# Optimization experiments

Hardware: AMD Instinct MI355X
Metric: run time of the kernel (lower is better)

## Reference

```python
import jax, jax.numpy as jnp
import numpy as np

B, H, W, C = 8, 64, 64, 512
C8, C2 = C // 8, C // 2  # f/g channels = 64, h channels = 256 (divisor = 2)


def _maxpool2x2(t):
    # [B, H, W, F] -> [B, H//2, W//2, F], valid 2x2 max pooling
    b, h, w, f = t.shape
    return t.reshape(b, h // 2, 2, w // 2, 2, f).max(axis=(2, 4))


def setup_inputs() -> dict:
    key = jax.random.key(0)
    kx, kf, kg, kh, ko, kgam = jax.random.split(key, 6)
    sf = lambda fan_in: (1.0 / np.sqrt(fan_in)).astype(np.float32)
    return {
        "x": jax.random.normal(kx, (B, H, W, C), dtype=jnp.float32),
        "wf": jax.random.normal(kf, (C, C8), dtype=jnp.float32) * sf(C),
        "wg": jax.random.normal(kg, (C, C8), dtype=jnp.float32) * sf(C),
        "wh": jax.random.normal(kh, (C, C2), dtype=jnp.float32) * sf(C),
        "wo": jax.random.normal(ko, (C2, C), dtype=jnp.float32) * sf(C2),
        "gamma": jax.random.normal(kgam, (1,), dtype=jnp.float32) * 0.1,
    }


def reference(x, wf, wg, wh, wo, gamma):
    b = x.shape[0]
    # 1x1 convs == channel matmuls
    f = _maxpool2x2(jnp.einsum("bhwc,cd->bhwd", x, wf)).reshape(b, -1, C8)  # [B, N/4, C/8]
    g = jnp.einsum("bhwc,cd->bhwd", x, wg).reshape(b, -1, C8)               # [B, N,   C/8]
    s = jnp.einsum("bqd,bkd->bqk", g, f)                                     # unscaled scores
    beta = jax.nn.softmax(s, axis=-1)
    h = _maxpool2x2(jnp.einsum("bhwc,cd->bhwd", x, wh)).reshape(b, -1, C2)  # [B, N/4, C/2]
    o = jnp.einsum("bqk,bkd->bqd", beta, h).reshape(b, H, W, C2)
    o = jnp.einsum("bhwd,dc->bhwc", o, wo)                                   # o_conv back to C
    return gamma * o + x
```

## Files before the change

kernel.cpp:

```cpp
#include <hip/hip_runtime.h>
#include <hip/hip_bf16.h>

#define NTOK 4096
#define NPOOL 1024

using short8 = __attribute__((ext_vector_type(8))) short;
using f32x4  = __attribute__((ext_vector_type(4))) float;

__device__ __forceinline__ unsigned short f2bf(float f) {
  __hip_bfloat16 h = __float2bfloat16(f);
  return __builtin_bit_cast(unsigned short, h);
}

__device__ __forceinline__ int pool_row(int bx, int m) {
  int pg = bx * 16 + (m >> 2);
  int corner = m & 3;
  int batch = pg >> 10;
  int pl = pg & 1023;
  int pi = pl >> 5, pj = pl & 31;
  return (batch << 12) + ((2 * pi + (corner >> 1)) << 6) + 2 * pj + (corner & 1);
}

__global__ __launch_bounds__(256) void pack_w(const float* __restrict__ wf,
                                              const float* __restrict__ wg,
                                              const float* __restrict__ wh,
                                              const float* __restrict__ wo,
                                              unsigned short* __restrict__ wcatT,
                                              unsigned short* __restrict__ woT) {
  int i = blockIdx.x * 256 + threadIdx.x;
  if (i < 384 * 512) {
    int n = i >> 9, k = i & 511;
    float v = (n < 64) ? wf[k * 64 + n]
            : (n < 128) ? wg[k * 64 + (n - 64)]
                        : wh[k * 256 + (n - 128)];
    wcatT[i] = f2bf(v);
  } else if (i < 384 * 512 + 512 * 256) {
    int j = i - 384 * 512;
    int n = j >> 8, k = j & 255;
    woT[j] = f2bf(wo[(size_t)k * 512 + n]);
  }
}

__global__ __launch_bounds__(512) void fgh_proj(const float* __restrict__ x,
                                                const unsigned short* __restrict__ wcatT,
                                                unsigned short* __restrict__ fB,
                                                unsigned short* __restrict__ gB,
                                                unsigned short* __restrict__ hT) {
  __shared__ unsigned short lds[17920];
  const int tid = threadIdx.x;
  const int bx = blockIdx.x;
  const int wave = tid >> 6, lane = tid & 63;
  const int col = lane & 15, rgrp = lane >> 4;
  const int wcol = wave * 48;

  f32x4 acc[4][3];
#pragma unroll
  for (int mt = 0; mt < 4; ++mt)
#pragma unroll
    for (int nt = 0; nt < 3; ++nt) acc[mt][nt] = (f32x4){0.f, 0.f, 0.f, 0.f};

  for (int kt = 0; kt < 16; ++kt) {
    __syncthreads();
    {
      int m = tid >> 3, k4 = (tid & 7) << 2;
      float4 v = *(const float4*)(x + (size_t)pool_row(bx, m) * 512 + kt * 32 + k4);
      ushort4 o4;
      o4.x = f2bf(v.x); o4.y = f2bf(v.y); o4.z = f2bf(v.z); o4.w = f2bf(v.w);
      *(ushort4*)&lds[m * 40 + k4] = o4;
    }
#pragma unroll
    for (int r = 0; r < 3; ++r) {
      int idx = tid + r * 512;
      int n = idx >> 2, k8 = (idx & 3) << 3;
      *(uint4*)&lds[2560 + n * 40 + k8] =
          *(const uint4*)(wcatT + (size_t)n * 512 + kt * 32 + k8);
    }
    __syncthreads();

    short8 am[4];
#pragma unroll
    for (int mt = 0; mt < 4; ++mt)
      am[mt] = *(const short8*)&lds[(mt * 16 + col) * 40 + rgrp * 8];
#pragma unroll
    for (int nt = 0; nt < 3; ++nt) {
      short8 bn = *(const short8*)&lds[2560 + (wcol + nt * 16 + col) * 40 + rgrp * 8];
#pragma unroll
      for (int mt = 0; mt < 4; ++mt)
        acc[mt][nt] = __builtin_amdgcn_mfma_f32_16x16x32_bf16(am[mt], bn, acc[mt][nt], 0, 0, 0);
    }
  }
  __syncthreads();

  unsigned short* gO = lds;
  unsigned short* fO = lds + 4608;
  unsigned short* hO = lds + 5760;
#pragma unroll
  for (int mt = 0; mt < 4; ++mt) {
#pragma unroll
    for (int nt = 0; nt < 3; ++nt) {
      int n = wcol + nt * 16 + col;
      f32x4 a = acc[mt][nt];
      if (n < 64) {
        float mx = fmaxf(fmaxf(a[0], a[1]), fmaxf(a[2], a[3]));
        fO[(mt * 4 + rgrp) * 72 + n] = f2bf(mx);
      } else if (n < 128) {
#pragma unroll
        for (int reg = 0; reg < 4; ++reg)
          gO[(mt * 16 + rgrp * 4 + reg) * 72 + (n - 64)] = f2bf(a[reg]);
      } else {
        float mx = fmaxf(fmaxf(a[0], a[1]), fmaxf(a[2], a[3]));
        hO[(n - 128) * 24 + (mt * 4 + rgrp)] = f2bf(mx);
      }
    }
  }
  __syncthreads();

  const int b = bx >> 6, pkb = (bx & 63) * 16;
  {
    int m = tid >> 3, d8 = (tid & 7) << 3;
    *(uint4*)(gB + (size_t)pool_row(bx, m) * 64 + d8) = *(const uint4*)&gO[m * 72 + d8];
  }
  if (tid < 128) {
    int pr = tid >> 3, d8 = (tid & 7) << 3;
    *(uint4*)(fB + (size_t)(bx * 16 + pr) * 64 + d8) = *(const uint4*)&fO[pr * 72 + d8];
  }
  {
    int dv = tid >> 1, p8 = (tid & 1) << 3;
    *(uint4*)(hT + (((size_t)b * 256 + dv) << 10) + pkb + p8) = *(const uint4*)&hO[dv * 24 + p8];
  }
}

__global__ __launch_bounds__(512) void attn_mfma(const __hip_bfloat16* __restrict__ G,
                                                 const __hip_bfloat16* __restrict__ F,
                                                 const __hip_bfloat16* __restrict__ HT,
                                                 unsigned short* __restrict__ O) {
  __shared__ unsigned short lds[33792];

  const int tid = threadIdx.x;
  const int wave = tid >> 6, lane = tid & 63;
  const int col = lane & 15;
  const int rgrp = lane >> 4;
  const int b = blockIdx.x >> 5, qt = blockIdx.x & 31;

  const unsigned short* Gb = (const unsigned short*)G + ((size_t)b * NTOK + qt * 128) * 64;
  const unsigned short* Fb = (const unsigned short*)F + (size_t)b * NPOOL * 64;
  const unsigned short* Hb = (const unsigned short*)HT + (size_t)b * 256 * NPOOL;

  short8 ag[2];
#pragma unroll
  for (int ks = 0; ks < 2; ++ks)
    ag[ks] = *(const short8*)(Gb + (size_t)(wave * 16 + col) * 64 + ks * 32 + rgrp * 8);

  f32x4 oacc[16];
#pragma unroll
  for (int t = 0; t < 16; ++t) oacc[t] = (f32x4){0.f, 0.f, 0.f, 0.f};
  float m_run[4], l_run[4];
#pragma unroll
  for (int r = 0; r < 4; ++r) { m_run[r] = -1e30f; l_run[r] = 0.f; }

  const int fk = tid >> 3, fd8 = (tid & 7) << 3;

  for (int kc = 0; kc < 16; ++kc) {
    __syncthreads();
    *(uint4*)&lds[fk * 72 + fd8] =
        *(const uint4*)(Fb + (size_t)(kc * 64 + fk) * 64 + fd8);
#pragma unroll
    for (int r = 0; r < 4; ++r) {
      int j = tid + r * 512;
      int dv = j >> 3, k8 = (j & 7) << 3;
      *(uint4*)&lds[4608 + dv * 72 + k8] =
          *(const uint4*)(Hb + (size_t)dv * NPOOL + kc * 64 + k8);
    }
    __syncthreads();

    f32x4 s[4];
#pragma unroll
    for (int t = 0; t < 4; ++t) s[t] = (f32x4){0.f, 0.f, 0.f, 0.f};
#pragma unroll
    for (int ks = 0; ks < 2; ++ks) {
#pragma unroll
      for (int t = 0; t < 4; ++t) {
        short8 bf = *(const short8*)&lds[(t * 16 + col) * 72 + ks * 32 + rgrp * 8];
        s[t] = __builtin_amdgcn_mfma_f32_16x16x32_bf16(ag[ks], bf, s[t], 0, 0, 0);
      }
    }

    float cm[4];
#pragma unroll
    for (int r = 0; r < 4; ++r) {
      cm[r] = fmaxf(fmaxf(s[0][r], s[1][r]), fmaxf(s[2][r], s[3][r]));
#pragma unroll
      for (int msk = 1; msk < 16; msk <<= 1) cm[r] = fmaxf(cm[r], __shfl_xor(cm[r], msk));
    }
    bool upd = false;
#pragma unroll
    for (int r = 0; r < 4; ++r) upd |= (cm[r] > m_run[r]);
    if (__any(upd)) {
      float alpha[4];
#pragma unroll
      for (int r = 0; r < 4; ++r) {
        float mn = fmaxf(m_run[r], cm[r]);
        alpha[r] = __expf(m_run[r] - mn);
        m_run[r] = mn;
        l_run[r] *= alpha[r];
      }
#pragma unroll
      for (int t = 0; t < 16; ++t) {
#pragma unroll
        for (int r = 0; r < 4; ++r) oacc[t][r] *= alpha[r];
      }
    }

    float rs[4] = {0.f, 0.f, 0.f, 0.f};
    const int prow = wave * 16 + rgrp * 4;
#pragma unroll
    for (int t = 0; t < 4; ++t) {
#pragma unroll
      for (int r = 0; r < 4; ++r) {
        float p = __expf(s[t][r] - m_run[r]);
        rs[r] += p;
        lds[23040 + (prow + r) * 72 + t * 16 + col] = f2bf(p);
      }
    }
#pragma unroll
    for (int r = 0; r < 4; ++r) {
#pragma unroll
      for (int msk = 1; msk < 16; msk <<= 1) rs[r] += __shfl_xor(rs[r], msk);
      l_run[r] += rs[r];
    }

    short8 ap[2];
#pragma unroll
    for (int ks = 0; ks < 2; ++ks)
      ap[ks] = *(const short8*)&lds[23040 + (wave * 16 + col) * 72 + ks * 32 + rgrp * 8];
#pragma unroll
    for (int t = 0; t < 16; ++t) {
#pragma unroll
      for (int ks = 0; ks < 2; ++ks) {
        short8 bh = *(const short8*)&lds[4608 + (t * 16 + col) * 72 + ks * 32 + rgrp * 8];
        oacc[t] = __builtin_amdgcn_mfma_f32_16x16x32_bf16(ap[ks], bh, oacc[t], 0, 0, 0);
      }
    }
  }

  float inv[4];
#pragma unroll
  for (int r = 0; r < 4; ++r) inv[r] = 1.0f / l_run[r];
  __syncthreads();
  const int qrow = wave * 16 + rgrp * 4;
#pragma unroll
  for (int t = 0; t < 16; ++t) {
#pragma unroll
    for (int r = 0; r < 4; ++r)
      lds[(qrow + r) * 264 + t * 16 + col] = f2bf(oacc[t][r] * inv[r]);
  }
  __syncthreads();
  unsigned short* Ob = O + ((size_t)b * NTOK + qt * 128) * 256;
#pragma unroll
  for (int r = 0; r < 8; ++r) {
    int idx = tid + r * 512;
    int q = idx >> 5, d8 = (idx & 31) << 3;
    *(uint4*)(Ob + (size_t)q * 256 + d8) = *(const uint4*)&lds[q * 264 + d8];
  }
}

__global__ __launch_bounds__(512) void gemm_out_mfma(const unsigned short* __restrict__ Obf,
                                                     const unsigned short* __restrict__ woT,
                                                     const float* __restrict__ Xres,
                                                     const float* __restrict__ gamma,
                                                     float* __restrict__ Out) {
  __shared__ unsigned short lds[23040];
  const int tid = threadIdx.x;
  const int bx = blockIdx.x;
  const int wave = tid >> 6, lane = tid & 63;
  const int col = lane & 15, rgrp = lane >> 4;
  const int wc = wave * 64;

  f32x4 acc[4][4];
#pragma unroll
  for (int mt = 0; mt < 4; ++mt)
#pragma unroll
    for (int nt = 0; nt < 4; ++nt) acc[mt][nt] = (f32x4){0.f, 0.f, 0.f, 0.f};

  for (int kt = 0; kt < 8; ++kt) {
    __syncthreads();
    if (tid < 256) {
      int m = tid >> 2, k8 = (tid & 3) << 3;
      *(uint4*)&lds[m * 40 + k8] =
          *(const uint4*)(Obf + ((size_t)bx * 64 + m) * 256 + kt * 32 + k8);
    }
#pragma unroll
    for (int r = 0; r < 4; ++r) {
      int idx = tid + r * 512;
      int n = idx >> 2, k8 = (idx & 3) << 3;
      *(uint4*)&lds[2560 + n * 40 + k8] =
          *(const uint4*)(woT + (size_t)n * 256 + kt * 32 + k8);
    }
    __syncthreads();

    short8 am[4];
#pragma unroll
    for (int mt = 0; mt < 4; ++mt)
      am[mt] = *(const short8*)&lds[(mt * 16 + col) * 40 + rgrp * 8];
#pragma unroll
    for (int nt = 0; nt < 4; ++nt) {
      short8 bn = *(const short8*)&lds[2560 + (wc + nt * 16 + col) * 40 + rgrp * 8];
#pragma unroll
      for (int mt = 0; mt < 4; ++mt)
        acc[mt][nt] = __builtin_amdgcn_mfma_f32_16x16x32_bf16(am[mt], bn, acc[mt][nt], 0, 0, 0);
    }
  }

  float gm = gamma[0];
#pragma unroll
  for (int mt = 0; mt < 4; ++mt) {
#pragma unroll
    for (int nt = 0; nt < 4; ++nt) {
      int n = wc + nt * 16 + col;
#pragma unroll
      for (int reg = 0; reg < 4; ++reg) {
        size_t row = (size_t)bx * 64 + mt * 16 + rgrp * 4 + reg;
        size_t off = row * 512 + n;
        Out[off] = gm * acc[mt][nt][reg] + Xres[off];
      }
    }
  }
}

extern "C" void kernel_launch(void* const* d_in, const int* in_sizes, int n_in,
                              void* d_out, int out_size, void* d_ws, size_t ws_size,
                              hipStream_t stream) {
  (void)in_sizes; (void)n_in; (void)out_size; (void)ws_size;
  const float* x     = (const float*)d_in[0];
  const float* wf    = (const float*)d_in[1];
  const float* wg    = (const float*)d_in[2];
  const float* wh    = (const float*)d_in[3];
  const float* wo    = (const float*)d_in[4];
  const float* gamma = (const float*)d_in[5];
  float* out = (float*)d_out;

  unsigned short* ws = (unsigned short*)d_ws;
  unsigned short* oB    = ws;
  unsigned short* gB    = ws + 8388608;
  unsigned short* fB    = ws + 10485760;
  unsigned short* hT    = ws + 11010048;
  unsigned short* wcatT = ws + 13107200;
  unsigned short* woT   = ws + 13303808;

  pack_w<<<1280, dim3(256), 0, stream>>>(wf, wg, wh, wo, wcatT, woT);
  fgh_proj<<<512, dim3(512), 0, stream>>>(x, wcatT, fB, gB, hT);
  attn_mfma<<<256, dim3(512), 0, stream>>>((const __hip_bfloat16*)gB, (const __hip_bfloat16*)fB,
                                           (const __hip_bfloat16*)hT, oB);
  gemm_out_mfma<<<512, dim3(512), 0, stream>>>(oB, woT, x, gamma, out);
}
```

Before: 226.0 us.

## Double-buffer LDS tiles with register prefetch in projection and attention kernels

Both the fgh projection and the flash-attention kernels now keep two LDS buffers. Each iteration issues the global loads for the next tile into registers before the MFMA work, then writes them to the other buffer afterwards, so one barrier per iteration replaces two. The goal is to hide global memory latency behind compute. In exchange, LDS use roughly doubles (attention goes to about 108KB) and register pressure rises, which may cut occupancy.

```diff
diff --git a/kernel.cpp b/kernel.cpp
--- a/kernel.cpp
+++ b/kernel.cpp
@@ -46,13 +46,38 @@
                                                 unsigned short* __restrict__ fB,
                                                 unsigned short* __restrict__ gB,
                                                 unsigned short* __restrict__ hT) {
-  __shared__ unsigned short lds[17920];
+  __shared__ unsigned short lds[35840];
   const int tid = threadIdx.x;
   const int bx = blockIdx.x;
   const int wave = tid >> 6, lane = tid & 63;
   const int col = lane & 15, rgrp = lane >> 4;
   const int wcol = wave * 48;
 
+  const int xm = tid >> 3, xk4 = (tid & 7) << 2;
+  const float* xsrc = x + (size_t)pool_row(bx, xm) * 512 + xk4;
+  const int xdst = xm * 40 + xk4;
+  int wsrc[3], wdst[3];
+#pragma unroll
+  for (int r = 0; r < 3; ++r) {
+    int idx = tid + r * 512;
+    int n = idx >> 2, k8 = (idx & 3) << 3;
+    wsrc[r] = n * 512 + k8;
+    wdst[r] = 2560 + n * 40 + k8;
+  }
+
+  float4 rx = *(const float4*)xsrc;
+  uint4 rw[3];
+#pragma unroll
+  for (int r = 0; r < 3; ++r) rw[r] = *(const uint4*)(wcatT + wsrc[r]);
+  {
+    ushort4 o4;
+    o4.x = f2bf(rx.x); o4.y = f2bf(rx.y); o4.z = f2bf(rx.z); o4.w = f2bf(rx.w);
+    *(ushort4*)&lds[xdst] = o4;
+  }
+#pragma unroll
+  for (int r = 0; r < 3; ++r) *(uint4*)&lds[wdst[r]] = rw[r];
+  __syncthreads();
+
   f32x4 acc[4][3];
 #pragma unroll
   for (int mt = 0; mt < 4; ++mt)
@@ -60,36 +85,35 @@
     for (int nt = 0; nt < 3; ++nt) acc[mt][nt] = (f32x4){0.f, 0.f, 0.f, 0.f};
 
   for (int kt = 0; kt < 16; ++kt) {
-    __syncthreads();
-    {
-      int m = tid >> 3, k4 = (tid & 7) << 2;
-      float4 v = *(const float4*)(x + (size_t)pool_row(bx, m) * 512 + kt * 32 + k4);
-      ushort4 o4;
-      o4.x = f2bf(v.x); o4.y = f2bf(v.y); o4.z = f2bf(v.z); o4.w = f2bf(v.w);
-      *(ushort4*)&lds[m * 40 + k4] = o4;
-    }
-#pragma unroll
-    for (int r = 0; r < 3; ++r) {
-      int idx = tid + r * 512;
-      int n = idx >> 2, k8 = (idx & 3) << 3;
-      *(uint4*)&lds[2560 + n * 40 + k8] =
-          *(const uint4*)(wcatT + (size_t)n * 512 + kt * 32 + k8);
-    }
-    __syncthreads();
+    const int cur = (kt & 1) * 17920;
+    const int nxt = 17920 - cur;
+    if (kt < 15) {
+      rx = *(const float4*)(xsrc + (kt + 1) * 32);
+#pragma unroll
+      for (int r = 0; r < 3; ++r) rw[r] = *(const uint4*)(wcatT + wsrc[r] + (kt + 1) * 32);
+    }
 
     short8 am[4];
 #pragma unroll
     for (int mt = 0; mt < 4; ++mt)
-      am[mt] = *(const short8*)&lds[(mt * 16 + col) * 40 + rgrp * 8];
+      am[mt] = *(const short8*)&lds[cur + (mt * 16 + col) * 40 + rgrp * 8];
 #pragma unroll
     for (int nt = 0; nt < 3; ++nt) {
-      short8 bn = *(const short8*)&lds[2560 + (wcol + nt * 16 + col) * 40 + rgrp * 8];
+      short8 bn = *(const short8*)&lds[cur + 2560 + (wcol + nt * 16 + col) * 40 + rgrp * 8];
 #pragma unroll
       for (int mt = 0; mt < 4; ++mt)
         acc[mt][nt] = __builtin_amdgcn_mfma_f32_16x16x32_bf16(am[mt], bn, acc[mt][nt], 0, 0, 0);
     }
-  }
-  __syncthreads();
+
+    if (kt < 15) {
+      ushort4 o4;
+      o4.x = f2bf(rx.x); o4.y = f2bf(rx.y); o4.z = f2bf(rx.z); o4.w = f2bf(rx.w);
+      *(ushort4*)&lds[nxt + xdst] = o4;
+#pragma unroll
+      for (int r = 0; r < 3; ++r) *(uint4*)&lds[nxt + wdst[r]] = rw[r];
+    }
+    __syncthreads();
+  }
 
   unsigned short* gO = lds;
   unsigned short* fO = lds + 4608;
@@ -134,7 +158,7 @@
                                                  const __hip_bfloat16* __restrict__ F,
                                                  const __hip_bfloat16* __restrict__ HT,
                                                  unsigned short* __restrict__ O) {
-  __shared__ unsigned short lds[33792];
+  __shared__ unsigned short lds[55296];
 
   const int tid = threadIdx.x;
   const int wave = tid >> 6, lane = tid & 63;
@@ -151,6 +175,27 @@
   for (int ks = 0; ks < 2; ++ks)
     ag[ks] = *(const short8*)(Gb + (size_t)(wave * 16 + col) * 64 + ks * 32 + rgrp * 8);
 
+  const int fk = tid >> 3, fd8 = (tid & 7) << 3;
+  const int fdst = fk * 72 + fd8;
+  const int fsrc = fk * 64 + fd8;
+  int hdst[4], hsrc[4];
+#pragma unroll
+  for (int r = 0; r < 4; ++r) {
+    int j = tid + r * 512;
+    int dv = j >> 3, k8 = (j & 7) << 3;
+    hdst[r] = 4608 + dv * 72 + k8;
+    hsrc[r] = dv * NPOOL + k8;
+  }
+
+  uint4 rf = *(const uint4*)(Fb + fsrc);
+  uint4 rh[4];
+#pragma unroll
+  for (int r = 0; r < 4; ++r) rh[r] = *(const uint4*)(Hb + hsrc[r]);
+  *(uint4*)&lds[fdst] = rf;
+#pragma unroll
+  for (int r = 0; r < 4; ++r) *(uint4*)&lds[hdst[r]] = rh[r];
+  __syncthreads();
+
   f32x4 oacc[16];
 #pragma unroll
   for (int t = 0; t < 16; ++t) oacc[t] = (f32x4){0.f, 0.f, 0.f, 0.f};
@@ -158,20 +203,14 @@
 #pragma unroll
   for (int r = 0; r < 4; ++r) { m_run[r] = -1e30f; l_run[r] = 0.f; }
 
-  const int fk = tid >> 3, fd8 = (tid & 7) << 3;
-
   for (int kc = 0; kc < 16; ++kc) {
-    __syncthreads();
-    *(uint4*)&lds[fk * 72 + fd8] =
-        *(const uint4*)(Fb + (size_t)(kc * 64 + fk) * 64 + fd8);
-#pragma unroll
-    for (int r = 0; r < 4; ++r) {
-      int j = tid + r * 512;
-      int dv = j >> 3, k8 = (j & 7) << 3;
-      *(uint4*)&lds[4608 + dv * 72 + k8] =
-          *(const uint4*)(Hb + (size_t)dv * NPOOL + kc * 64 + k8);
-    }
-    __syncthreads();
+    const int cur = (kc & 1) * 23040;
+    const int nxt = 23040 - cur;
+    if (kc < 15) {
+      rf = *(const uint4*)(Fb + (kc + 1) * 4096 + fsrc);
+#pragma unroll
+      for (int r = 0; r < 4; ++r) rh[r] = *(const uint4*)(Hb + (kc + 1) * 64 + hsrc[r]);
+    }
 
     f32x4 s[4];
 #pragma unroll
@@ -180,7 +219,7 @@
     for (int ks = 0; ks < 2; ++ks) {
 #pragma unroll
       for (int t = 0; t < 4; ++t) {
-        short8 bf = *(const short8*)&lds[(t * 16 + col) * 72 + ks * 32 + rgrp * 8];
+        short8 bf = *(const short8*)&lds[cur + (t * 16 + col) * 72 + ks * 32 + rgrp * 8];
         s[t] = __builtin_amdgcn_mfma_f32_16x16x32_bf16(ag[ks], bf, s[t], 0, 0, 0);
       }
     }
@@ -219,7 +258,7 @@
       for (int r = 0; r < 4; ++r) {
         float p = __expf(s[t][r] - m_run[r]);
         rs[r] += p;
-        lds[23040 + (prow + r) * 72 + t * 16 + col] = f2bf(p);
+        lds[46080 + (prow + r) * 72 + t * 16 + col] = f2bf(p);
       }
     }
 #pragma unroll
@@ -232,21 +271,27 @@
     short8 ap[2];
 #pragma unroll
     for (int ks = 0; ks < 2; ++ks)
-      ap[ks] = *(const short8*)&lds[23040 + (wave * 16 + col) * 72 + ks * 32 + rgrp * 8];
+      ap[ks] = *(const short8*)&lds[46080 + (wave * 16 + col) * 72 + ks * 32 + rgrp * 8];
 #pragma unroll
     for (int t = 0; t < 16; ++t) {
 #pragma unroll
       for (int ks = 0; ks < 2; ++ks) {
-        short8 bh = *(const short8*)&lds[4608 + (t * 16 + col) * 72 + ks * 32 + rgrp * 8];
+        short8 bh = *(const short8*)&lds[cur + 4608 + (t * 16 + col) * 72 + ks * 32 + rgrp * 8];
         oacc[t] = __builtin_amdgcn_mfma_f32_16x16x32_bf16(ap[ks], bh, oacc[t], 0, 0, 0);
       }
     }
+
+    if (kc < 15) {
+      *(uint4*)&lds[nxt + fdst] = rf;
+#pragma unroll
+      for (int r = 0; r < 4; ++r) *(uint4*)&lds[nxt + hdst[r]] = rh[r];
+    }
+    __syncthreads();
   }
 
   float inv[4];
 #pragma unroll
   for (int r = 0; r < 4; ++r) inv[r] = 1.0f / l_run[r];
-  __syncthreads();
   const int qrow = wave * 16 + rgrp * 4;
 #pragma unroll
   for (int t = 0; t < 16; ++t) {
```

Measured after the change: 254.2 us. 1.12x slower.

## Stage full A tile in LDS once and read weights directly from global

Applied to the files above, without the earlier changes.

In both projection GEMMs, the whole K extent of the activation tile is loaded into LDS once up front, replacing a per-k-tile load with two barriers per iteration. Weight fragments are read straight from global memory into MFMA operands, relying on cache since each wave reads distinct columns. This removes most barriers and LDS staging for weights. In exchange it uses more LDS in fgh_proj, which may lower occupancy, and the weight reads are uncoalesced 16-byte per-lane global loads.

```diff
diff --git a/kernel.cpp b/kernel.cpp
--- a/kernel.cpp
+++ b/kernel.cpp
@@ -46,44 +46,41 @@
                                                 unsigned short* __restrict__ fB,
                                                 unsigned short* __restrict__ gB,
                                                 unsigned short* __restrict__ hT) {
-  __shared__ unsigned short lds[17920];
+  __shared__ unsigned short lds[33280];
   const int tid = threadIdx.x;
   const int bx = blockIdx.x;
   const int wave = tid >> 6, lane = tid & 63;
   const int col = lane & 15, rgrp = lane >> 4;
   const int wcol = wave * 48;
 
-  f32x4 acc[4][3];
-#pragma unroll
-  for (int mt = 0; mt < 4; ++mt)
-#pragma unroll
-    for (int nt = 0; nt < 3; ++nt) acc[mt][nt] = (f32x4){0.f, 0.f, 0.f, 0.f};
-
-  for (int kt = 0; kt < 16; ++kt) {
-    __syncthreads();
-    {
-      int m = tid >> 3, k4 = (tid & 7) << 2;
-      float4 v = *(const float4*)(x + (size_t)pool_row(bx, m) * 512 + kt * 32 + k4);
+  {
+    const int xm = tid >> 3, xk4 = (tid & 7) << 2;
+    const float* xrow = x + (size_t)pool_row(bx, xm) * 512 + xk4;
+    unsigned short* dst = &lds[xm * 520 + xk4];
+#pragma unroll
+    for (int kt = 0; kt < 16; ++kt) {
+      float4 v = *(const float4*)(xrow + kt * 32);
       ushort4 o4;
       o4.x = f2bf(v.x); o4.y = f2bf(v.y); o4.z = f2bf(v.z); o4.w = f2bf(v.w);
-      *(ushort4*)&lds[m * 40 + k4] = o4;
-    }
-#pragma unroll
-    for (int r = 0; r < 3; ++r) {
-      int idx = tid + r * 512;
-      int n = idx >> 2, k8 = (idx & 3) << 3;
-      *(uint4*)&lds[2560 + n * 40 + k8] =
-          *(const uint4*)(wcatT + (size_t)n * 512 + kt * 32 + k8);
-    }
-    __syncthreads();
-
+      *(ushort4*)(dst + kt * 32) = o4;
+    }
+  }
+  __syncthreads();
+
+  f32x4 acc[4][3];
+#pragma unroll
+  for (int mt = 0; mt < 4; ++mt)
+#pragma unroll
+    for (int nt = 0; nt < 3; ++nt) acc[mt][nt] = (f32x4){0.f, 0.f, 0.f, 0.f};
+
+  for (int kt = 0; kt < 16; ++kt) {
     short8 am[4];
 #pragma unroll
     for (int mt = 0; mt < 4; ++mt)
-      am[mt] = *(const short8*)&lds[(mt * 16 + col) * 40 + rgrp * 8];
+      am[mt] = *(const short8*)&lds[(mt * 16 + col) * 520 + kt * 32 + rgrp * 8];
 #pragma unroll
     for (int nt = 0; nt < 3; ++nt) {
-      short8 bn = *(const short8*)&lds[2560 + (wcol + nt * 16 + col) * 40 + rgrp * 8];
+      short8 bn = *(const short8*)(wcatT + (size_t)(wcol + nt * 16 + col) * 512 + kt * 32 + rgrp * 8);
 #pragma unroll
       for (int mt = 0; mt < 4; ++mt)
         acc[mt][nt] = __builtin_amdgcn_mfma_f32_16x16x32_bf16(am[mt], bn, acc[mt][nt], 0, 0, 0);
@@ -269,13 +266,22 @@
                                                      const float* __restrict__ Xres,
                                                      const float* __restrict__ gamma,
                                                      float* __restrict__ Out) {
-  __shared__ unsigned short lds[23040];
+  __shared__ unsigned short lds[16896];
   const int tid = threadIdx.x;
   const int bx = blockIdx.x;
   const int wave = tid >> 6, lane = tid & 63;
   const int col = lane & 15, rgrp = lane >> 4;
   const int wc = wave * 64;
 
+#pragma unroll
+  for (int r = 0; r < 4; ++r) {
+    int idx = tid + r * 512;
+    int m = idx >> 5, k8 = (idx & 31) << 3;
+    *(uint4*)&lds[m * 264 + k8] =
+        *(const uint4*)(Obf + ((size_t)bx * 64 + m) * 256 + k8);
+  }
+  __syncthreads();
+
   f32x4 acc[4][4];
 #pragma unroll
   for (int mt = 0; mt < 4; ++mt)
@@ -283,28 +289,13 @@
     for (int nt = 0; nt < 4; ++nt) acc[mt][nt] = (f32x4){0.f, 0.f, 0.f, 0.f};
 
   for (int kt = 0; kt < 8; ++kt) {
-    __syncthreads();
-    if (tid < 256) {
-      int m = tid >> 2, k8 = (tid & 3) << 3;
-      *(uint4*)&lds[m * 40 + k8] =
-          *(const uint4*)(Obf + ((size_t)bx * 64 + m) * 256 + kt * 32 + k8);
-    }
-#pragma unroll
-    for (int r = 0; r < 4; ++r) {
-      int idx = tid + r * 512;
-      int n = idx >> 2, k8 = (idx & 3) << 3;
-      *(uint4*)&lds[2560 + n * 40 + k8] =
-          *(const uint4*)(woT + (size_t)n * 256 + kt * 32 + k8);
-    }
-    __syncthreads();
-
     short8 am[4];
 #pragma unroll
     for (int mt = 0; mt < 4; ++mt)
-      am[mt] = *(const short8*)&lds[(mt * 16 + col) * 40 + rgrp * 8];
+      am[mt] = *(const short8*)&lds[(mt * 16 + col) * 264 + kt * 32 + rgrp * 8];
 #pragma unroll
     for (int nt = 0; nt < 4; ++nt) {
-      short8 bn = *(const short8*)&lds[2560 + (wc + nt * 16 + col) * 40 + rgrp * 8];
+      short8 bn = *(const short8*)(woT + (size_t)(wc + nt * 16 + col) * 256 + kt * 32 + rgrp * 8);
 #pragma unroll
       for (int mt = 0; mt < 4; ++mt)
         acc[mt][nt] = __builtin_amdgcn_mfma_f32_16x16x32_bf16(am[mt], bn, acc[mt][nt], 0, 0, 0);
```

After: 229.2 us. About the same (+1.4%).
